# Performance work log

Measured on AMD Instinct MI355X. Metric: run time of the kernel, lower is better.

Reference implementation:

```python
import jax, jax.numpy as jnp
import numpy as np

B, N_PATTS, D_PATTS, L_PATTS, L_SEQ = 32, 32, 12, 32, 1024
L_OUT = 32
RHO = 1.0
BIG = 1e30  # stands in for +inf at DP boundaries (finite to keep grads clean)


def setup_inputs() -> dict:
    key = jax.random.key(0)
    kx, kp = jax.random.split(key)
    x = jax.random.normal(kx, (B, D_PATTS, L_SEQ), dtype=jnp.float32)
    patts = jax.random.normal(kp, (N_PATTS, D_PATTS, L_PATTS), dtype=jnp.float32)
    return {"x": x, "patts": patts}


def _pairwise_sqdist(x, patts):
    # cost[b,n,i,j] = sum_d (patts[n,d,i] - x[b,d,j])^2, shape [B,N,P,L]
    x2 = jnp.sum(x * x, axis=1)            # [B,L]
    p2 = jnp.sum(patts * patts, axis=1)    # [N,P]
    cross = jnp.einsum('bdl,ndp->bnpl', x, patts)  # [B,N,P,L]
    return p2[None, :, :, None] + x2[:, None, None, :] - 2.0 * cross


def _dp_column(a, c, w):
    # Solve cur[i] = c[i] + min(a[i], w*cur[i-1]) sequentially over pattern axis.
    # a, c: [B,N,P]; returns [B,N,P]
    a_t = jnp.moveaxis(a, -1, 0)  # [P,B,N]
    c_t = jnp.moveaxis(c, -1, 0)

    def step(cur_prev, ac):
        a_i, c_i = ac
        cur = c_i + jnp.minimum(a_i, w * cur_prev)
        return cur, cur

    init = jnp.full(c.shape[:-1], BIG, c.dtype)  # no row above the first
    _, cur = jax.lax.scan(step, init, (a_t, c_t))
    return jnp.moveaxis(cur, 0, -1)


def _dtw_dp(cost, w):
    # Weighted DTW recurrence:
    #   D[i,j] = cost[i,j] + min(D[i-1,j-1], w*D[i-1,j], w*D[i,j-1])
    # with D[0,0] = cost[0,0] and out-of-range predecessors = +inf.
    # cost: [B,N,P,L] -> D: [B,N,P,L]
    Bb, Nn, P, L = cost.shape
    cost_t = jnp.moveaxis(cost, -1, 0)  # [L,B,N,P]

    # first column j=0: D[i,0] = c[i,0] + w*D[i-1,0], D[0,0] = c[0,0]
    a0 = jnp.where(jnp.arange(P) == 0, 0.0, BIG).astype(cost.dtype)
    a0 = jnp.broadcast_to(a0, cost.shape[:3])
    d0 = _dp_column(a0, cost_t[0], w)  # [B,N,P]

    def outer_step(d_prev, c_col):
        # prev_shift[i] = D[i-1, j-1]; boundary row is +inf for j >= 1
        top = jnp.full_like(d_prev[..., :1], BIG)
        prev_shift = jnp.concatenate([top, d_prev[..., :-1]], axis=-1)
        a = jnp.minimum(prev_shift, w * d_prev)
        cur = _dp_column(a, c_col, w)
        return cur, cur

    _, rest = jax.lax.scan(outer_step, d0, cost_t[1:])  # [L-1,B,N,P]
    D = jnp.concatenate([d0[None], rest], axis=0)       # [L,B,N,P]
    return jnp.moveaxis(D, 0, -1)                       # [B,N,P,L]


def reference(x, patts):
    w = RHO ** (1.0 / L_PATTS)
    cost = _pairwise_sqdist(x, patts)   # [B,N,P,L]
    D = _dtw_dp(cost, w)                # [B,N,P,L]
    return D[..., -L_OUT:]              # [B,N,P,L_OUT]
```

## Files before the change

kernel.cpp:

```cpp
#include <hip/hip_runtime.h>


#define BIGF 1e30f
#define LL   1024
#define LOUT 32

using v4f = __attribute__((ext_vector_type(4))) float;
using v2f = __attribute__((ext_vector_type(2))) float;

__device__ __forceinline__ v2f fma2(v2f a, v2f b, v2f c) {
    return __builtin_elementwise_fma(a, b, c);
}
__device__ __forceinline__ v2f bc2(float s) { v2f r = {s, s}; return r; }

template<int CTRL>
__device__ __forceinline__ float dpp_self(float v) {
    return __int_as_float(__builtin_amdgcn_update_dpp(
        __float_as_int(v), __float_as_int(v), CTRL, 0xF, 0xF, false));
}
template<int CTRL>
__device__ __forceinline__ float dpp_zero(float v) {
    return __int_as_float(__builtin_amdgcn_update_dpp(
        0, __float_as_int(v), CTRL, 0xF, 0xF, false));
}
__device__ __forceinline__ float wshr1z(float v) {
    return __int_as_float(__builtin_amdgcn_update_dpp(
        0, __float_as_int(v), 0x138 , 0xF, 0xF, false));
}
__device__ __forceinline__ float rdlane(float v, int l) {
    return __int_as_float(__builtin_amdgcn_readlane(__float_as_int(v), l));
}

__device__ __forceinline__ float scan_min64_fast(float t, int lane) {
    t = fminf(t, dpp_self<0x111>(t));
    t = fminf(t, dpp_self<0x112>(t));
    t = fminf(t, dpp_self<0x114>(t));
    t = fminf(t, dpp_self<0x118>(t));
    float r0 = rdlane(t, 15), r1 = rdlane(t, 31), r2 = rdlane(t, 47);
    t = fminf(t, (lane >= 16) ? r0 : BIGF);
    t = fminf(t, (lane >= 32) ? r1 : BIGF);
    t = fminf(t, (lane >= 48) ? r2 : BIGF);
    return t;
}
__device__ __forceinline__ float scan_add64_dpp(float t, int lane) {
    t += dpp_zero<0x111>(t);
    t += dpp_zero<0x112>(t);
    t += dpp_zero<0x114>(t);
    t += dpp_zero<0x118>(t);
    float r0 = rdlane(t, 15), r1 = rdlane(t, 31), r2 = rdlane(t, 47);
    t += (lane >= 16) ? r0 : 0.0f;
    t += (lane >= 32) ? r1 : 0.0f;
    t += (lane >= 48) ? r2 : 0.0f;
    return t;
}

__global__ __launch_bounds__(64)
__attribute__((amdgpu_waves_per_eu(1, 1)))
void dtw_kernel(const float* __restrict__ x, const float* __restrict__ patts,
                float* __restrict__ out) {
    const int lane = threadIdx.x;
    const bool l0  = (lane == 0);
    const int blk  = blockIdx.x;
    const int b    = blk >> 5, n = blk & 31;
    const float* __restrict__ xb = x + b * (12 * LL);
    const float* __restrict__ pn = patts + n * (12 * 32);

    float prm[12], p2r;
    {
        const int r = lane & 31;
        float s2 = 0.f;
#pragma unroll
        for (int d = 0; d < 12; ++d) {
            float v = pn[d * 32 + r];
            s2 = fmaf(v, v, s2);
            prm[d] = -2.0f * v;
        }
        p2r = s2;
    }

    v2f SXp[12][8];
#pragma unroll
    for (int d = 0; d < 12; ++d) {
#pragma unroll
        for (int c = 0; c < 4; ++c) {
            v4f v = *(const v4f*)(xb + d * LL + 16 * lane + 4 * c);
            v2f lo = {v.x, v.y}, hi = {v.z, v.w};
            SXp[d][2 * c]     = lo;
            SXp[d][2 * c + 1] = hi;
        }
    }
    v2f SX2p[8];
#pragma unroll
    for (int j = 0; j < 8; ++j) {
        v2f t = SXp[0][j] * SXp[0][j];
#pragma unroll
        for (int d = 1; d < 12; ++d) t = fma2(SXp[d][j], SXp[d][j], t);
        SX2p[j] = t;
    }
#pragma unroll
    for (int d = 0; d < 12; ++d) {
        float run = 0.f;
#pragma unroll
        for (int j = 0; j < 8; ++j) {
            float a0 = SXp[d][j].x + run;
            float a1 = SXp[d][j].y + a0;
            SXp[d][j].x = a0; SXp[d][j].y = a1; run = a1;
        }
        float ex = scan_add64_dpp(run, lane) - run;
        v2f exv = bc2(ex);
#pragma unroll
        for (int j = 0; j < 8; ++j) SXp[d][j] += exv;
    }
    {
        float run = 0.f;
#pragma unroll
        for (int j = 0; j < 8; ++j) {
            float a0 = SX2p[j].x + run;
            float a1 = SX2p[j].y + a0;
            SX2p[j].x = a0; SX2p[j].y = a1; run = a1;
        }
        float ex = scan_add64_dpp(run, lane) - run;
        v2f exv = bc2(ex);
#pragma unroll
        for (int j = 0; j < 8; ++j) SX2p[j] += exv;
    }
    v2f jp1p[8];
#pragma unroll
    for (int j = 0; j < 8; ++j) {
        v2f t = {(float)(16 * lane + 2 * j + 1), (float)(16 * lane + 2 * j + 2)};
        jp1p[j] = t;
    }

    v2f S2[8];
    float Dp[16];
    {
        float pv[12], p2u;
#pragma unroll
        for (int d = 0; d < 12; ++d) pv[d] = rdlane(prm[d], 0);
        p2u = rdlane(p2r, 0);
#pragma unroll
        for (int j = 0; j < 8; ++j) S2[j] = fma2(bc2(p2u), jp1p[j], SX2p[j]);
#pragma unroll
        for (int d = 0; d < 12; ++d)
#pragma unroll
            for (int j = 0; j < 8; ++j) S2[j] = fma2(bc2(pv[d]), SXp[d][j], S2[j]);
#pragma unroll
        for (int k = 0; k < 16; ++k) Dp[k] = S2[k >> 1][k & 1];
        if (lane >= 62) {
            float* ob = out + blk * (32 * LOUT) + (lane - 62) * 16;
#pragma unroll
            for (int c = 0; c < 4; ++c) {
                v4f v = {Dp[4*c], Dp[4*c+1], Dp[4*c+2], Dp[4*c+3]};
                *(v4f*)(ob + 4 * c) = v;
            }
        }
    }

#pragma unroll 2
    for (int i = 1; i < 32; ++i) {
        float pv[12], p2u;
#pragma unroll
        for (int d = 0; d < 12; ++d) pv[d] = rdlane(prm[d], i);
        p2u = rdlane(p2r, i);

#pragma unroll
        for (int j = 0; j < 8; ++j) S2[j] = fma2(bc2(p2u), jp1p[j], SX2p[j]);
#pragma unroll
        for (int d = 0; d < 12; ++d)
#pragma unroll
            for (int j = 0; j < 8; ++j) S2[j] = fma2(bc2(pv[d]), SXp[d][j], S2[j]);

        float dsh = wshr1z(Dp[15]); dsh = l0 ? BIGF : dsh;
        float se  = wshr1z(S2[7].y);

        float m[16];
        m[0] = fminf(dsh, Dp[0]) - se;
#pragma unroll
        for (int k = 1; k < 16; ++k)
            m[k] = fminf(m[k-1],
                         fminf(Dp[k-1], Dp[k]) - S2[(k-1) >> 1][(k-1) & 1]);

        float t  = scan_min64_fast(m[15], lane);
        float te = wshr1z(t); te = l0 ? BIGF : te;

#pragma unroll
        for (int k = 0; k < 16; ++k)
            Dp[k] = S2[k >> 1][k & 1] + fminf(te, m[k]);

        if (lane >= 62) {
            float* ob = out + blk * (32 * LOUT) + (lane - 62) * 16;
#pragma unroll
            for (int c = 0; c < 4; ++c) {
                v4f v = {Dp[4*c], Dp[4*c+1], Dp[4*c+2], Dp[4*c+3]};
                *(v4f*)(ob + i * 32 + 4 * c) = v;
            }
        }
    }
}

extern "C" void kernel_launch(void* const* d_in, const int* in_sizes, int n_in,
                              void* d_out, int out_size, void* d_ws, size_t ws_size,
                              hipStream_t stream) {
    const float* x     = (const float*)d_in[0];
    const float* patts = (const float*)d_in[1];
    float* out         = (float*)d_out;
    dtw_kernel<<<dim3(1024), dim3(64), 0, stream>>>(x, patts, out);
}
```

Baseline: 77.70 us.

## Split DTW columns across two wavefronts with LDS-handoff wavefront pipeline

Measured after the change: 80.94 us. +4.2%, slower.

```diff
diff --git a/kernel.cpp b/kernel.cpp
--- a/kernel.cpp
+++ b/kernel.cpp
@@ -54,17 +54,23 @@
     return t;
 }
 
-__global__ __launch_bounds__(64)
-__attribute__((amdgpu_waves_per_eu(1, 1)))
+__global__ __launch_bounds__(128, 2)
 void dtw_kernel(const float* __restrict__ x, const float* __restrict__ patts,
                 float* __restrict__ out) {
-    const int lane = threadIdx.x;
+    const int tid  = threadIdx.x;
+    const int lane = tid & 63;
+    const int wv   = tid >> 6;
     const bool l0  = (lane == 0);
     const int blk  = blockIdx.x;
     const int b    = blk >> 5, n = blk & 31;
     const float* __restrict__ xb = x + b * (12 * LL);
     const float* __restrict__ pn = patts + n * (12 * 32);
 
+    __shared__ float ldsZ[32];
+    __shared__ float ldsS[32];
+    __shared__ float ldsD[32];
+    __shared__ float ldsT[16];
+
     float prm[12], p2r;
     {
         const int r = lane & 31;
@@ -78,20 +84,21 @@
         p2r = s2;
     }
 
-    v2f SXp[12][8];
+    const int colbase = (wv << 9) + (lane << 3);
+    v2f SXp[12][4];
 #pragma unroll
     for (int d = 0; d < 12; ++d) {
 #pragma unroll
-        for (int c = 0; c < 4; ++c) {
-            v4f v = *(const v4f*)(xb + d * LL + 16 * lane + 4 * c);
+        for (int c = 0; c < 2; ++c) {
+            v4f v = *(const v4f*)(xb + d * LL + colbase + 4 * c);
             v2f lo = {v.x, v.y}, hi = {v.z, v.w};
             SXp[d][2 * c]     = lo;
             SXp[d][2 * c + 1] = hi;
         }
     }
-    v2f SX2p[8];
-#pragma unroll
-    for (int j = 0; j < 8; ++j) {
+    v2f SX2p[4];
+#pragma unroll
+    for (int j = 0; j < 4; ++j) {
         v2f t = SXp[0][j] * SXp[0][j];
 #pragma unroll
         for (int d = 1; d < 12; ++d) t = fma2(SXp[d][j], SXp[d][j], t);
@@ -101,100 +108,145 @@
     for (int d = 0; d < 12; ++d) {
         float run = 0.f;
 #pragma unroll
-        for (int j = 0; j < 8; ++j) {
+        for (int j = 0; j < 4; ++j) {
             float a0 = SXp[d][j].x + run;
             float a1 = SXp[d][j].y + a0;
             SXp[d][j].x = a0; SXp[d][j].y = a1; run = a1;
         }
-        float ex = scan_add64_dpp(run, lane) - run;
-        v2f exv = bc2(ex);
-#pragma unroll
-        for (int j = 0; j < 8; ++j) SXp[d][j] += exv;
+        float inc = scan_add64_dpp(run, lane);
+        if (wv == 0 && lane == 63) ldsT[d] = inc;
+        v2f exv = bc2(inc - run);
+#pragma unroll
+        for (int j = 0; j < 4; ++j) SXp[d][j] += exv;
     }
     {
         float run = 0.f;
 #pragma unroll
-        for (int j = 0; j < 8; ++j) {
+        for (int j = 0; j < 4; ++j) {
             float a0 = SX2p[j].x + run;
             float a1 = SX2p[j].y + a0;
             SX2p[j].x = a0; SX2p[j].y = a1; run = a1;
         }
-        float ex = scan_add64_dpp(run, lane) - run;
-        v2f exv = bc2(ex);
-#pragma unroll
-        for (int j = 0; j < 8; ++j) SX2p[j] += exv;
-    }
-    v2f jp1p[8];
-#pragma unroll
-    for (int j = 0; j < 8; ++j) {
-        v2f t = {(float)(16 * lane + 2 * j + 1), (float)(16 * lane + 2 * j + 2)};
+        float inc = scan_add64_dpp(run, lane);
+        if (wv == 0 && lane == 63) ldsT[12] = inc;
+        v2f exv = bc2(inc - run);
+#pragma unroll
+        for (int j = 0; j < 4; ++j) SX2p[j] += exv;
+    }
+    __syncthreads();
+    if (wv == 1) {
+#pragma unroll
+        for (int d = 0; d < 12; ++d) {
+            v2f t = bc2(ldsT[d]);
+#pragma unroll
+            for (int j = 0; j < 4; ++j) SXp[d][j] += t;
+        }
+        v2f t2 = bc2(ldsT[12]);
+#pragma unroll
+        for (int j = 0; j < 4; ++j) SX2p[j] += t2;
+    }
+
+    v2f jp1p[4];
+#pragma unroll
+    for (int j = 0; j < 4; ++j) {
+        v2f t = {(float)(colbase + 2 * j + 1), (float)(colbase + 2 * j + 2)};
         jp1p[j] = t;
     }
 
-    v2f S2[8];
-    float Dp[16];
-    {
-        float pv[12], p2u;
-#pragma unroll
-        for (int d = 0; d < 12; ++d) pv[d] = rdlane(prm[d], 0);
-        p2u = rdlane(p2r, 0);
-#pragma unroll
-        for (int j = 0; j < 8; ++j) S2[j] = fma2(bc2(p2u), jp1p[j], SX2p[j]);
-#pragma unroll
-        for (int d = 0; d < 12; ++d)
-#pragma unroll
-            for (int j = 0; j < 8; ++j) S2[j] = fma2(bc2(pv[d]), SXp[d][j], S2[j]);
-#pragma unroll
-        for (int k = 0; k < 16; ++k) Dp[k] = S2[k >> 1][k & 1];
-        if (lane >= 62) {
-            float* ob = out + blk * (32 * LOUT) + (lane - 62) * 16;
-#pragma unroll
-            for (int c = 0; c < 4; ++c) {
-                v4f v = {Dp[4*c], Dp[4*c+1], Dp[4*c+2], Dp[4*c+3]};
-                *(v4f*)(ob + 4 * c) = v;
+    v2f S2[4];
+    float Dp[8];
+
+#define COMPUTE_S(i) do { \
+    float pv[12], p2u; \
+    _Pragma("unroll") for (int d = 0; d < 12; ++d) pv[d] = rdlane(prm[d], (i)); \
+    p2u = rdlane(p2r, (i)); \
+    _Pragma("unroll") for (int j = 0; j < 4; ++j) \
+        S2[j] = fma2(bc2(p2u), jp1p[j], SX2p[j]); \
+    _Pragma("unroll") for (int d = 0; d < 12; ++d) { \
+        v2f pb = bc2(pv[d]); \
+        _Pragma("unroll") for (int j = 0; j < 4; ++j) \
+            S2[j] = fma2(pb, SXp[d][j], S2[j]); \
+    } \
+} while (0)
+
+#define ROW0() do { \
+    COMPUTE_S(0); \
+    _Pragma("unroll") for (int k = 0; k < 8; ++k) Dp[k] = S2[k >> 1][k & 1]; \
+} while (0)
+
+#define STORE_ROW(i) do { \
+    if (lane >= 60) { \
+        float* ob = out + blk * (32 * LOUT) + (i) * LOUT + (lane - 60) * 8; \
+        v4f va = {Dp[0], Dp[1], Dp[2], Dp[3]}; \
+        v4f vb = {Dp[4], Dp[5], Dp[6], Dp[7]}; \
+        *(v4f*)ob = va; *(v4f*)(ob + 4) = vb; \
+    } \
+} while (0)
+
+#define ROW_W0(i) do { \
+    COMPUTE_S(i); \
+    float dsh = wshr1z(Dp[7]); dsh = l0 ? BIGF : dsh; \
+    float se  = wshr1z(S2[3].y);               \
+    float m[8]; \
+    m[0] = fminf(dsh, Dp[0]) - se; \
+    _Pragma("unroll") for (int k = 1; k < 8; ++k) \
+        m[k] = fminf(m[k-1], \
+                     fminf(Dp[k-1], Dp[k]) - S2[(k-1) >> 1][(k-1) & 1]); \
+    float t = scan_min64_fast(m[7], lane); \
+    float te = wshr1z(t); te = l0 ? BIGF : te; \
+    _Pragma("unroll") for (int k = 0; k < 8; ++k) \
+        Dp[k] = S2[k >> 1][k & 1] + fminf(te, m[k]); \
+    if (lane == 63) { ldsZ[i] = t; ldsS[i] = S2[3].y; ldsD[i] = Dp[7]; } \
+} while (0)
+
+#define ROW_W1(i, Z0, Sb, Db) do { \
+    COMPUTE_S(i); \
+    float dsh = wshr1z(Dp[7]); dsh = l0 ? (Db) : dsh; \
+    float se  = wshr1z(S2[3].y); se = l0 ? (Sb) : se; \
+    float m[8]; \
+    m[0] = fminf(dsh, Dp[0]) - se; \
+    _Pragma("unroll") for (int k = 1; k < 8; ++k) \
+        m[k] = fminf(m[k-1], \
+                     fminf(Dp[k-1], Dp[k]) - S2[(k-1) >> 1][(k-1) & 1]); \
+    float t = scan_min64_fast(m[7], lane); \
+    float te = wshr1z(t); te = l0 ? BIGF : te; \
+    te = fminf(te, (Z0)); \
+    _Pragma("unroll") for (int k = 0; k < 8; ++k) \
+        Dp[k] = S2[k >> 1][k & 1] + fminf(te, m[k]); \
+    STORE_ROW(i); \
+} while (0)
+
+    if (wv == 0) {
+        ROW0();
+        if (lane == 63) { ldsZ[0] = BIGF; ldsS[0] = S2[3].y; ldsD[0] = Dp[7]; }
+        ROW_W0(1);
+    }
+    __syncthreads();
+    for (int kk = 1; kk < 16; ++kk) {
+        if (wv == 0) {
+            ROW_W0(2 * kk);
+            ROW_W0(2 * kk + 1);
+        } else {
+            const int i0 = 2 * kk - 2, i1 = 2 * kk - 1;
+            if (kk == 1) {
+                ROW0();
+                STORE_ROW(0);
+                float Z0b = ldsZ[1], Sbb = ldsS[1], Dbb = ldsD[0];
+                ROW_W1(1, Z0b, Sbb, Dbb);
+            } else {
+                float Z0a = ldsZ[i0], Sba = ldsS[i0], Dba = ldsD[i0 - 1];
+                float Z0b = ldsZ[i1], Sbb = ldsS[i1], Dbb = ldsD[i1 - 1];
+                ROW_W1(i0, Z0a, Sba, Dba);
+                ROW_W1(i1, Z0b, Sbb, Dbb);
             }
         }
-    }
-
-#pragma unroll 2
-    for (int i = 1; i < 32; ++i) {
-        float pv[12], p2u;
-#pragma unroll
-        for (int d = 0; d < 12; ++d) pv[d] = rdlane(prm[d], i);
-        p2u = rdlane(p2r, i);
-
-#pragma unroll
-        for (int j = 0; j < 8; ++j) S2[j] = fma2(bc2(p2u), jp1p[j], SX2p[j]);
-#pragma unroll
-        for (int d = 0; d < 12; ++d)
-#pragma unroll
-            for (int j = 0; j < 8; ++j) S2[j] = fma2(bc2(pv[d]), SXp[d][j], S2[j]);
-
-        float dsh = wshr1z(Dp[15]); dsh = l0 ? BIGF : dsh;
-        float se  = wshr1z(S2[7].y);
-
-        float m[16];
-        m[0] = fminf(dsh, Dp[0]) - se;
-#pragma unroll
-        for (int k = 1; k < 16; ++k)
-            m[k] = fminf(m[k-1],
-                         fminf(Dp[k-1], Dp[k]) - S2[(k-1) >> 1][(k-1) & 1]);
-
-        float t  = scan_min64_fast(m[15], lane);
-        float te = wshr1z(t); te = l0 ? BIGF : te;
-
-#pragma unroll
-        for (int k = 0; k < 16; ++k)
-            Dp[k] = S2[k >> 1][k & 1] + fminf(te, m[k]);
-
-        if (lane >= 62) {
-            float* ob = out + blk * (32 * LOUT) + (lane - 62) * 16;
-#pragma unroll
-            for (int c = 0; c < 4; ++c) {
-                v4f v = {Dp[4*c], Dp[4*c+1], Dp[4*c+2], Dp[4*c+3]};
-                *(v4f*)(ob + i * 32 + 4 * c) = v;
-            }
-        }
+        __syncthreads();
+    }
+    if (wv == 1) {
+        float Z0a = ldsZ[30], Sba = ldsS[30], Dba = ldsD[29];
+        float Z0b = ldsZ[31], Sbb = ldsS[31], Dbb = ldsD[30];
+        ROW_W1(30, Z0a, Sba, Dba);
+        ROW_W1(31, Z0b, Sbb, Dbb);
     }
 }
 
@@ -204,5 +256,5 @@
     const float* x     = (const float*)d_in[0];
     const float* patts = (const float*)d_in[1];
     float* out         = (float*)d_out;
-    dtw_kernel<<<dim3(1024), dim3(64), 0, stream>>>(x, patts, out);
-}
+    dtw_kernel<<<dim3(1024), dim3(128), 0, stream>>>(x, patts, out);
+}
```
